# Optimization experiments

Measured on AMD Instinct MI355X. Metric: run time of the kernel, lower is better.

Reference implementation:

```python
import jax, jax.numpy as jnp
import numpy as np

B, G, D, N_HEADS, FFN, L = 16, 2048, 256, 8, 1024, 4
HEAD_DIM = D // N_HEADS
EPS_LN = 1e-5
MASK_TOKEN = -10.0
REE_BASE = 100.0


def setup_inputs() -> dict:
    key = jax.random.key(0)
    ks = jax.random.split(key, 20)
    s = 0.02
    inp = {
        'x': jax.random.normal(ks[0], (B, G), jnp.float32),
        'gene_emb': jax.random.normal(ks[1], (G, D), jnp.float32) * s,
        'inv_freq': (1.0 / REE_BASE ** (jnp.arange(0, D, 2, dtype=jnp.float32) / D)),
        'Wq': jax.random.normal(ks[2], (L, D, D), jnp.float32) * s,
        'bq': jnp.zeros((L, D), jnp.float32),
        'Wk': jax.random.normal(ks[3], (L, D, D), jnp.float32) * s,
        'bk': jnp.zeros((L, D), jnp.float32),
        'Wv': jax.random.normal(ks[4], (L, D, D), jnp.float32) * s,
        'bv': jnp.zeros((L, D), jnp.float32),
        'ln1_g': jnp.ones((L, D), jnp.float32),
        'ln1_b': jnp.zeros((L, D), jnp.float32),
        'ln2_g': jnp.ones((L, D), jnp.float32),
        'ln2_b': jnp.zeros((L, D), jnp.float32),
        'WU': jax.random.normal(ks[5], (L, D, FFN), jnp.float32) * s,
        'bU': jnp.zeros((L, FFN), jnp.float32),
        'WV': jax.random.normal(ks[6], (L, FFN, D), jnp.float32) * s,
        'bV': jnp.zeros((L, D), jnp.float32),
        'Wout': jax.random.normal(ks[7], (D, 1), jnp.float32) * s,
        'bout': jnp.zeros((1,), jnp.float32),
    }
    return inp


def layernorm(x, g, b):
    m = x.mean(-1, keepdims=True)
    v = ((x - m) ** 2).mean(-1, keepdims=True)
    return (x - m) / jnp.sqrt(v + EPS_LN) * g + b


def causal_linear_attention(q, k, v):
    # q, k already feature-mapped ('sqr'); shapes [B, S, H, dh]
    b, s, h, dh = q.shape
    qs, ks_, vs = (jnp.moveaxis(t, 1, 0) for t in (q, k, v))  # [S,B,H,dh]
    num0 = jnp.zeros((b, h, dh, dh), q.dtype)
    den0 = jnp.zeros((b, h, dh), q.dtype)

    def step(carry, qkv):
        num_s, den_s = carry
        qt, kt, vt = qkv
        num_s = num_s + jnp.einsum('bhf,bhd->bhfd', kt, vt)
        den_s = den_s + kt
        num = jnp.einsum('bhf,bhfd->bhd', qt, num_s)
        den = jnp.einsum('bhf,bhf->bh', qt, den_s)
        return (num_s, den_s), num / (den[..., None] + 1e-16)

    _, out = jax.lax.scan(step, (num0, den0), (qs, ks_, vs))  # [S,B,H,dh]
    return jnp.moveaxis(out, 0, 1).reshape(b, s, h * dh)


def reference(x, gene_emb, inv_freq, Wq, bq, Wk, bk, Wv, bv,
              ln1_g, ln1_b, ln2_g, ln2_b, WU, bU, WV, bV, Wout, bout):
    b, g = x.shape
    # Rotary Expression Embedding
    freqs = x[..., None] * inv_freq  # [B,G,D/2]
    emb = jnp.concatenate([jnp.sin(freqs), jnp.cos(freqs)], axis=-1)  # [B,G,D]
    emb = jnp.where((x == MASK_TOKEN)[..., None], 0.0, emb)
    h = gene_emb[None] + emb  # [B,G,D]

    for l in range(Wq.shape[0]):
        hn = layernorm(h, ln1_g[l], ln1_b[l])  # pre-LN (on_gptln=True)
        q = (hn @ Wq[l] + bq[l]).reshape(b, g, N_HEADS, HEAD_DIM) ** 2
        k = (hn @ Wk[l] + bk[l]).reshape(b, g, N_HEADS, HEAD_DIM) ** 2
        v = (hn @ Wv[l] + bv[l]).reshape(b, g, N_HEADS, HEAD_DIM)
        h = h + causal_linear_attention(q, k, v)
        hn2 = layernorm(h, ln2_g[l], ln2_b[l])
        h = h + jax.nn.gelu(hn2 @ WU[l] + bU[l], approximate=False) @ WV[l] + bV[l]
    return (h @ Wout + bout).squeeze(-1)  # [B,G]
```

## Files before the change

kernel.cpp:

```cpp
#include <hip/hip_runtime.h>
#include <math.h>


#define GG 2048
#define DD 256
#define NROWS 32768
#define NC 32
#define CS 64

typedef __attribute__((ext_vector_type(8))) short bf16x8;
typedef __attribute__((ext_vector_type(4))) float f32x4;

__device__ __forceinline__ short f2bf(float f) {
  union { float f; unsigned u; } v; v.f = f;
  unsigned r = v.u + 0x7FFFu + ((v.u >> 16) & 1u);
  return (short)(r >> 16);
}
__device__ __forceinline__ float bf2f(short s) {
  union { unsigned u; float f; } v; v.u = ((unsigned)(unsigned short)s) << 16;
  return v.f;
}
__device__ __forceinline__ void gld16(const short* g, short* l) {
  __builtin_amdgcn_global_load_lds(
      (const __attribute__((address_space(1))) void*)g,
      (__attribute__((address_space(3))) void*)l, 16, 0, 0);
}
__device__ __forceinline__ float fast_gelu(float x) {
  float y = 1.595769122f * (x + 0.044715f * x * x * x);
  return x / (1.0f + __expf(-y));
}

__global__ __launch_bounds__(256) void embed_kernel(
    const float* __restrict__ x, const float* __restrict__ ge,
    const float* __restrict__ invf, float* __restrict__ h) {
  int bg = blockIdx.x * 4 + (threadIdx.x >> 6);
  int g = bg & (GG - 1);
  int lane = threadIdx.x & 63;
  float xv = x[bg];
  int d = lane * 4;
  float4 e;
  if (lane < 32) {
    float4 f = *(const float4*)&invf[d];
    e.x = sinf(xv * f.x); e.y = sinf(xv * f.y);
    e.z = sinf(xv * f.z); e.w = sinf(xv * f.w);
  } else {
    float4 f = *(const float4*)&invf[d - 128];
    e.x = cosf(xv * f.x); e.y = cosf(xv * f.y);
    e.z = cosf(xv * f.z); e.w = cosf(xv * f.w);
  }
  if (xv == -10.0f) { e.x = 0.f; e.y = 0.f; e.z = 0.f; e.w = 0.f; }
  float4 gv = *(const float4*)&ge[(size_t)g * DD + d];
  float4 o; o.x = gv.x + e.x; o.y = gv.y + e.y; o.z = gv.z + e.z; o.w = gv.w + e.w;
  *(float4*)&h[(size_t)bg * DD + d] = o;
}

__global__ __launch_bounds__(256) void ln_tiled(
    const float* __restrict__ h, const float* __restrict__ gamma,
    const float* __restrict__ beta, short* __restrict__ outT) {
  __shared__ float mean_s[32], rstd_s[32];
  __shared__ float gls[256], bls[256];
  int r0 = blockIdx.x * 32;
  int tid = threadIdx.x;
  gls[tid] = gamma[tid]; bls[tid] = beta[tid];
  {
    int row = tid >> 3, seg = tid & 7;
    const float4* hp = (const float4*)(h + (size_t)(r0 + row) * DD + seg * 32);
    float s = 0.f, s2 = 0.f;
#pragma unroll
    for (int i = 0; i < 8; ++i) {
      float4 v = hp[i];
      s += v.x + v.y + v.z + v.w;
      s2 += v.x * v.x + v.y * v.y + v.z * v.z + v.w * v.w;
    }
    s += __shfl_xor(s, 1); s += __shfl_xor(s, 2); s += __shfl_xor(s, 4);
    s2 += __shfl_xor(s2, 1); s2 += __shfl_xor(s2, 2); s2 += __shfl_xor(s2, 4);
    if (seg == 0) {
      float mn = s * (1.0f / 256.0f);
      mean_s[row] = mn;
      rstd_s[row] = rsqrtf(s2 * (1.0f / 256.0f) - mn * mn + 1e-5f);
    }
  }
  __syncthreads();
  int row = tid & 31, kc8 = (tid >> 5) & 3, half = tid >> 7;
  float mn = mean_s[row], rs = rstd_s[row];
  size_t hrow = (size_t)(r0 + row) * DD;
  int trow = (r0 & 127) + row;
  short* tb = outT + (size_t)(r0 >> 7) * 8 * 4096 + (kc8 * 128 + trow) * 8;
#pragma unroll
  for (int j = 0; j < 4; ++j) {
    int kb = half * 4 + j;
    int k0 = kb * 32 + kc8 * 8;
    float4 x0 = *(const float4*)&h[hrow + k0];
    float4 x1 = *(const float4*)&h[hrow + k0 + 4];
    float4 g0 = *(const float4*)&gls[k0], g1 = *(const float4*)&gls[k0 + 4];
    float4 b0 = *(const float4*)&bls[k0], b1 = *(const float4*)&bls[k0 + 4];
    bf16x8 aw;
    aw[0] = f2bf((x0.x - mn) * rs * g0.x + b0.x);
    aw[1] = f2bf((x0.y - mn) * rs * g0.y + b0.y);
    aw[2] = f2bf((x0.z - mn) * rs * g0.z + b0.z);
    aw[3] = f2bf((x0.w - mn) * rs * g0.w + b0.w);
    aw[4] = f2bf((x1.x - mn) * rs * g1.x + b1.x);
    aw[5] = f2bf((x1.y - mn) * rs * g1.y + b1.y);
    aw[6] = f2bf((x1.z - mn) * rs * g1.z + b1.z);
    aw[7] = f2bf((x1.w - mn) * rs * g1.w + b1.w);
    *(bf16x8*)&tb[(size_t)kb * 4096] = aw;
  }
}

__global__ __launch_bounds__(256) void prep_weights(
    const float* __restrict__ Wq, const float* __restrict__ Wk,
    const float* __restrict__ Wv, const float* __restrict__ WU,
    const float* __restrict__ WV,
    short* __restrict__ TQ, short* __restrict__ TK, short* __restrict__ TV,
    short* __restrict__ TU, short* __restrict__ TVd) {
  int zz = blockIdx.z, l = blockIdx.y;
  const float* src; short* dst; int Kd, Nd;
  if (zz == 0) { src = Wq; dst = TQ; Kd = 256; Nd = 256; }
  else if (zz == 1) { src = Wk; dst = TK; Kd = 256; Nd = 256; }
  else if (zz == 2) { src = Wv; dst = TV; Kd = 256; Nd = 256; }
  else if (zz == 3) { src = WU; dst = TU; Kd = 256; Nd = 1024; }
  else { src = WV; dst = TVd; Kd = 1024; Nd = 256; }
  int tot = Kd * Nd;
  int e = blockIdx.x * 256 + threadIdx.x;
  if (e >= tot) return;
  int t = e >> 12;
  int cslot = (e >> 3) & 511;
  int elem = e & 7;
  int kc8 = cslot >> 7, rn = cslot & 127;
  int nKb = Kd >> 5;
  int nt = t / nKb, kb = t - nt * nKb;
  int n = nt * 128 + rn, k = kb * 32 + kc8 * 8 + elem;
  dst[(size_t)l * tot + e] = f2bf(src[(size_t)l * tot + (size_t)k * Nd + n]);
}

__global__ __launch_bounds__(256) void gemm_qkv(
    const short* __restrict__ A, const short* __restrict__ B0,
    const short* __restrict__ B1, const short* __restrict__ B2,
    const float* __restrict__ bias0, const float* __restrict__ bias1,
    const float* __restrict__ bias2,
    short* __restrict__ o0, short* __restrict__ o1, short* __restrict__ o2) {
  __shared__ __align__(16) short L[24576];
  constexpr int nIter = 8;
  int z = blockIdx.z;
  const short* Bt = (z == 0) ? B0 : (z == 1) ? B1 : B2;
  const float* bias = (z == 0) ? bias0 : (z == 1) ? bias1 : bias2;
  short* outz = (z == 0) ? o0 : (z == 1) ? o1 : o2;
  int m0 = blockIdx.x * 128, n0 = blockIdx.y * 128;
  int tid = threadIdx.x;
  int lane = tid & 63, w = tid >> 6;
  int q = lane >> 4, r = lane & 15;
  int wm = (w >> 1) * 64, wn = (w & 1) * 64;
  const short* At = A + (size_t)blockIdx.x * nIter * 4096;
  const short* Btl = Bt + (size_t)blockIdx.y * nIter * 4096;
  f32x4 vzero = {0.f, 0.f, 0.f, 0.f};
  f32x4 acc[4][4];
#pragma unroll
  for (int i = 0; i < 4; ++i)
#pragma unroll
    for (int j = 0; j < 4; ++j) acc[i][j] = vzero;

  int c0 = tid * 8, c1 = (tid + 256) * 8;
#pragma unroll
  for (int g = 0; g < 3; ++g) {
    gld16(At + g * 4096 + c0, &L[g * 4096 + c0]);
    gld16(At + g * 4096 + c1, &L[g * 4096 + c1]);
    gld16(Btl + g * 4096 + c0, &L[12288 + g * 4096 + c0]);
    gld16(Btl + g * 4096 + c1, &L[12288 + g * 4096 + c1]);
  }
  int abase = (q * 128 + wm + r) * 8;
  int bbase = (q * 128 + wn + r) * 8;

#pragma unroll
  for (int gi = 0; gi < nIter; ++gi) {
    const int rem = nIter - 1 - gi;
    if (rem >= 2)      __builtin_amdgcn_s_waitcnt(0x0f78);
    else if (rem == 1) __builtin_amdgcn_s_waitcnt(0x0f74);
    else               __builtin_amdgcn_s_waitcnt(0x0f70);
    __builtin_amdgcn_s_barrier();
    const int cur = gi % 3;
    const short* Asc = &L[cur * 4096];
    const short* Bsc = &L[12288 + cur * 4096];
    bf16x8 af[4], bfr[4];
#pragma unroll
    for (int mt = 0; mt < 4; ++mt)
      af[mt] = *(const bf16x8*)&Asc[abase + mt * 16 * 8];
#pragma unroll
    for (int nt = 0; nt < 4; ++nt)
      bfr[nt] = *(const bf16x8*)&Bsc[bbase + nt * 16 * 8];
#pragma unroll
    for (int mt = 0; mt < 4; ++mt)
#pragma unroll
      for (int nt = 0; nt < 4; ++nt)
        acc[mt][nt] = __builtin_amdgcn_mfma_f32_16x16x32_bf16(bfr[nt], af[mt], acc[mt][nt], 0, 0, 0);
    __builtin_amdgcn_s_waitcnt(0xc07f);
    __builtin_amdgcn_s_barrier();
    if (gi + 3 < nIter) {
      size_t kn = (size_t)(gi + 3) * 4096;
      gld16(At + kn + c0, &L[cur * 4096 + c0]);
      gld16(At + kn + c1, &L[cur * 4096 + c1]);
      gld16(Btl + kn + c0, &L[12288 + cur * 4096 + c0]);
      gld16(Btl + kn + c1, &L[12288 + cur * 4096 + c1]);
    }
  }

  float4 bias4[4];
#pragma unroll
  for (int nt = 0; nt < 4; ++nt) bias4[nt] = *(const float4*)&bias[n0 + wn + nt * 16 + q * 4];
  short* T = L;
#pragma unroll
  for (int mt = 0; mt < 4; ++mt) {
    int ml = wm + mt * 16 + r;
#pragma unroll
    for (int nt = 0; nt < 4; ++nt) {
      f32x4 v = acc[mt][nt];
      v[0] += bias4[nt].x; v[1] += bias4[nt].y; v[2] += bias4[nt].z; v[3] += bias4[nt].w;
      if (z < 2) { v[0] *= v[0]; v[1] *= v[1]; v[2] *= v[2]; v[3] *= v[3]; }
      short4 pk; pk.x = f2bf(v[0]); pk.y = f2bf(v[1]); pk.z = f2bf(v[2]); pk.w = f2bf(v[3]);
      *(short4*)&T[ml * 132 + wn + nt * 16 + q * 4] = pk;
    }
  }
  __syncthreads();
#pragma unroll
  for (int t2 = 0; t2 < 2; ++t2) {
    int task = tid + t2 * 256;
    int row = task & 127, hl = task >> 7;
    size_t obase = ((size_t)((n0 >> 5) + hl) * NROWS + m0 + row) * 32;
#pragma unroll
    for (int j = 0; j < 4; ++j)
      *(bf16x8*)&outz[obase + j * 8] = *(const bf16x8*)&T[row * 132 + hl * 32 + j * 8];
  }
}

__global__ __launch_bounds__(256, 2) void ffn_fused(
    const short* __restrict__ hnT, const short* __restrict__ TU,
    const short* __restrict__ TVd,
    const float* __restrict__ bU, const float* __restrict__ bV,
    float* __restrict__ h) {
  __shared__ __align__(16) short S[21248];
  short* MID = &S[12288];
  int tid = threadIdx.x;
  int lane = tid & 63, w = tid >> 6;
  int q = lane >> 4, r = lane & 15;
  int m0 = blockIdx.x * 64;
  int wm1 = (w >> 1) * 32, wn1 = (w & 1) * 64;
  int wm2 = w * 16;
  const short* Abase = hnT + (size_t)(m0 >> 7) * 32768 +
                       ((tid >> 6) * 128 + (m0 & 127) + (tid & 63)) * 8;
  int c0 = tid * 8, c1 = (tid + 256) * 8;

  f32x4 vzero = {0.f, 0.f, 0.f, 0.f};
  f32x4 acc2[16];
#pragma unroll
  for (int i = 0; i < 16; ++i) acc2[i] = vzero;

  int ab1 = (q * 64 + wm1 + r) * 8;
  int bb1 = (q * 128 + wn1 + r) * 8;
  int ab2 = (wm2 + r) * 136 + q * 8;

  for (int f = 0; f < 8; ++f) {
    const short* Ub = TU + (size_t)f * 8 * 4096;
#pragma unroll
    for (int g = 0; g < 2; ++g) {
      gld16(Abase + g * 4096, &S[g * 2048 + tid * 8]);
      gld16(Ub + g * 4096 + c0, &S[4096 + g * 4096 + c0]);
      gld16(Ub + g * 4096 + c1, &S[4096 + g * 4096 + c1]);
    }
    f32x4 acc1[2][4];
#pragma unroll
    for (int i = 0; i < 2; ++i)
#pragma unroll
      for (int j = 0; j < 4; ++j) acc1[i][j] = vzero;
#pragma unroll
    for (int gi = 0; gi < 8; ++gi) {
      if (gi < 7) __builtin_amdgcn_s_waitcnt(0x0f73);
      else        __builtin_amdgcn_s_waitcnt(0x0f70);
      __builtin_amdgcn_s_barrier();
      const int cur = gi & 1;
      const short* Asc = &S[cur * 2048];
      const short* Bsc = &S[4096 + cur * 4096];
      bf16x8 af[2], bfr[4];
#pragma unroll
      for (int mt = 0; mt < 2; ++mt)
        af[mt] = *(const bf16x8*)&Asc[ab1 + mt * 16 * 8];
#pragma unroll
      for (int nt = 0; nt < 4; ++nt)
        bfr[nt] = *(const bf16x8*)&Bsc[bb1 + nt * 16 * 8];
#pragma unroll
      for (int mt = 0; mt < 2; ++mt)
#pragma unroll
        for (int nt = 0; nt < 4; ++nt)
          acc1[mt][nt] = __builtin_amdgcn_mfma_f32_16x16x32_bf16(bfr[nt], af[mt], acc1[mt][nt], 0, 0, 0);
      __builtin_amdgcn_s_waitcnt(0xc07f);
      __builtin_amdgcn_s_barrier();
      if (gi + 2 < 8) {
        size_t kn = (size_t)(gi + 2) * 4096;
        gld16(Abase + kn, &S[cur * 2048 + tid * 8]);
        gld16(Ub + kn + c0, &S[4096 + cur * 4096 + c0]);
        gld16(Ub + kn + c1, &S[4096 + cur * 4096 + c1]);
      }
    }
#pragma unroll
    for (int mt = 0; mt < 2; ++mt) {
      int ml = wm1 + mt * 16 + r;
#pragma unroll
      for (int nt = 0; nt < 4; ++nt) {
        int fl = wn1 + nt * 16 + q * 4;
        float4 bu4 = *(const float4*)&bU[f * 128 + fl];
        f32x4 v = acc1[mt][nt];
        v[0] = fast_gelu(v[0] + bu4.x); v[1] = fast_gelu(v[1] + bu4.y);
        v[2] = fast_gelu(v[2] + bu4.z); v[3] = fast_gelu(v[3] + bu4.w);
        short4 pk; pk.x = f2bf(v[0]); pk.y = f2bf(v[1]); pk.z = f2bf(v[2]); pk.w = f2bf(v[3]);
        *(short4*)&MID[ml * 136 + fl] = pk;
      }
    }
#pragma unroll
    for (int kb2 = 0; kb2 < 4; ++kb2) {
      const short* Vb0 = TVd + (size_t)(4 * f + kb2) * 4096;
      const short* Vb1 = Vb0 + (size_t)32 * 4096;
      gld16(Vb0 + c0, &S[4096 + c0]);
      gld16(Vb0 + c1, &S[4096 + c1]);
      gld16(Vb1 + c0, &S[8192 + c0]);
      gld16(Vb1 + c1, &S[8192 + c1]);
      __builtin_amdgcn_s_waitcnt(0x0070);
      __builtin_amdgcn_s_barrier();
      bf16x8 af1 = *(const bf16x8*)&MID[ab2 + kb2 * 32];
#pragma unroll
      for (int nt = 0; nt < 16; ++nt) {
        int tile = nt >> 3, nl = nt & 7;
        bf16x8 bfr = *(const bf16x8*)&S[4096 + tile * 4096 + (q * 128 + nl * 16 + r) * 8];
        acc2[nt] = __builtin_amdgcn_mfma_f32_16x16x32_bf16(bfr, af1, acc2[nt], 0, 0, 0);
      }
      __builtin_amdgcn_s_waitcnt(0xc07f);
      __builtin_amdgcn_s_barrier();
    }
  }

  float* TF = (float*)S;
  float4 bv4[16];
#pragma unroll
  for (int nt = 0; nt < 16; ++nt) bv4[nt] = *(const float4*)&bV[nt * 16 + q * 4];
#pragma unroll
  for (int half = 0; half < 2; ++half) {
    __syncthreads();
#pragma unroll
    for (int nt8 = 0; nt8 < 8; ++nt8) {
      int nt = half * 8 + nt8;
      f32x4 v = acc2[nt];
      v[0] += bv4[nt].x; v[1] += bv4[nt].y; v[2] += bv4[nt].z; v[3] += bv4[nt].w;
      *(f32x4*)&TF[(wm2 + r) * 132 + nt8 * 16 + q * 4] = v;
    }
    __syncthreads();
    int row = tid >> 2, seg = tid & 3;
    size_t hoff = (size_t)(m0 + row) * DD + half * 128 + seg * 32;
#pragma unroll
    for (int j = 0; j < 8; ++j) {
      float4 add = *(const float4*)&TF[row * 132 + seg * 32 + j * 4];
      float4 cur4 = *(float4*)&h[hoff + j * 4];
      cur4.x += add.x; cur4.y += add.y; cur4.z += add.z; cur4.w += add.w;
      *(float4*)&h[hoff + j * 4] = cur4;
    }
  }
}

__global__ __launch_bounds__(256) void attn_chunk_kv(
    const short* __restrict__ Kb, const short* __restrict__ Vb,
    float* __restrict__ St, float* __restrict__ Zc) {
  __shared__ short Kt[4][32 * 72];
  __shared__ short Vt[4][32 * 72];
  int wid = threadIdx.x >> 6;
  int blk = blockIdx.x * 4 + wid;
  int c = blk & (NC - 1), bh = blk >> 5;
  int b = bh >> 3, hh = bh & 7;
  int lane = threadIdx.x & 63, q = lane >> 4, r = lane & 15;
  size_t rowbase = ((size_t)hh * NROWS + b * GG + c * CS + lane) * 32;
#pragma unroll
  for (int j = 0; j < 4; ++j) {
    bf16x8 kv = *(const bf16x8*)&Kb[rowbase + j * 8];
    bf16x8 vv = *(const bf16x8*)&Vb[rowbase + j * 8];
#pragma unroll
    for (int e = 0; e < 8; ++e) {
      Kt[wid][(j * 8 + e) * 72 + lane] = kv[e];
      Vt[wid][(j * 8 + e) * 72 + lane] = vv[e];
    }
  }
  __syncthreads();
  f32x4 vzero = {0.f, 0.f, 0.f, 0.f};
  f32x4 acc[2][2];
#pragma unroll
  for (int i = 0; i < 2; ++i)
#pragma unroll
    for (int j = 0; j < 2; ++j) acc[i][j] = vzero;
#pragma unroll
  for (int ks = 0; ks < 2; ++ks) {
    bf16x8 afr[2], bfr[2];
#pragma unroll
    for (int mt = 0; mt < 2; ++mt) afr[mt] = *(const bf16x8*)&Kt[wid][(mt * 16 + r) * 72 + ks * 32 + q * 8];
#pragma unroll
    for (int nt = 0; nt < 2; ++nt) bfr[nt] = *(const bf16x8*)&Vt[wid][(nt * 16 + r) * 72 + ks * 32 + q * 8];
#pragma unroll
    for (int mt = 0; mt < 2; ++mt)
#pragma unroll
      for (int nt = 0; nt < 2; ++nt)
        acc[mt][nt] = __builtin_amdgcn_mfma_f32_16x16x32_bf16(afr[mt], bfr[nt], acc[mt][nt], 0, 0, 0);
  }
  float* stp = St + ((size_t)bh * NC + c) * 1024;
#pragma unroll
  for (int mt = 0; mt < 2; ++mt)
#pragma unroll
    for (int nt = 0; nt < 2; ++nt)
      *(f32x4*)&stp[(nt * 16 + r) * 32 + mt * 16 + q * 4] = acc[mt][nt];
  if (lane < 32) {
    float s = 0.f;
#pragma unroll
    for (int j = 0; j < 8; ++j) {
      bf16x8 kr = *(const bf16x8*)&Kt[wid][lane * 72 + j * 8];
#pragma unroll
      for (int e = 0; e < 8; ++e) s += bf2f(kr[e]);
    }
    Zc[((size_t)bh * NC + c) * 32 + lane] = s;
  }
}

__global__ __launch_bounds__(1024) void attn_prefix(float* __restrict__ St, float* __restrict__ Zc) {
  int bh = blockIdx.x, i = threadIdx.x;
  float run = 0.f;
  float* p = St + (size_t)bh * NC * 1024 + i;
#pragma unroll
  for (int c = 0; c < NC; ++c) { float t = p[(size_t)c * 1024]; p[(size_t)c * 1024] = run; run += t; }
  if (i < 32) {
    float rz = 0.f;
    float* pz = Zc + (size_t)bh * NC * 32 + i;
#pragma unroll
    for (int c = 0; c < NC; ++c) { float t = pz[c * 32]; pz[c * 32] = rz; rz += t; }
  }
}

__global__ __launch_bounds__(256) void attn_intra(
    const short* __restrict__ Qb, const short* __restrict__ Kb,
    const short* __restrict__ Vb, const float* __restrict__ St,
    const float* __restrict__ Zc, float* __restrict__ h) {
  __shared__ short P[4][64 * 72];
  __shared__ short Vt[4][32 * 72];
  __shared__ float den[4][64];
  int wid = threadIdx.x >> 6;
  int blk = blockIdx.x * 4 + wid;
  int c = blk & (NC - 1), bh = blk >> 5;
  int b = bh >> 3, hh = bh & 7;
  int lane = threadIdx.x & 63, q = lane >> 4, r = lane & 15;
  size_t hrow0 = (size_t)b * GG + c * CS;
  size_t qrow0 = (size_t)hh * NROWS + b * GG + c * CS;

  const float* zp = Zc + ((size_t)bh * NC + c) * 32;
  float qz = 0.f;
  {
    size_t qoff = (qrow0 + lane) * 32;
#pragma unroll
    for (int j = 0; j < 4; ++j) {
      bf16x8 qv = *(const bf16x8*)&Qb[qoff + j * 8];
#pragma unroll
      for (int e = 0; e < 8; ++e) qz += bf2f(qv[e]) * zp[j * 8 + e];
    }
  }
  den[wid][lane] = qz;
  {
    size_t voff = (qrow0 + lane) * 32;
#pragma unroll
    for (int j = 0; j < 4; ++j) {
      bf16x8 vv = *(const bf16x8*)&Vb[voff + j * 8];
#pragma unroll
      for (int e = 0; e < 8; ++e) Vt[wid][(j * 8 + e) * 72 + lane] = vv[e];
    }
  }
  bf16x8 ak[4], bqf[4];
#pragma unroll
  for (int t4 = 0; t4 < 4; ++t4) {
    ak[t4]  = *(const bf16x8*)&Kb[(qrow0 + t4 * 16 + r) * 32 + q * 8];
    bqf[t4] = *(const bf16x8*)&Qb[(qrow0 + t4 * 16 + r) * 32 + q * 8];
  }
  f32x4 vzero = {0.f, 0.f, 0.f, 0.f};
  f32x4 pacc[4][4];
#pragma unroll
  for (int mt = 0; mt < 4; ++mt)
#pragma unroll
    for (int nt = 0; nt < 4; ++nt)
      pacc[mt][nt] = __builtin_amdgcn_mfma_f32_16x16x32_bf16(ak[mt], bqf[nt], vzero, 0, 0, 0);

  float rs[4] = {0.f, 0.f, 0.f, 0.f};
#pragma unroll
  for (int nt = 0; nt < 4; ++nt) {
    int t = nt * 16 + r;
#pragma unroll
    for (int mt = 0; mt < 4; ++mt) {
      short4 pk;
#pragma unroll
      for (int rr = 0; rr < 4; ++rr) {
        int s = mt * 16 + q * 4 + rr;
        float pv = (s <= t) ? pacc[mt][nt][rr] : 0.f;
        rs[nt] += pv;
        ((short*)&pk)[rr] = f2bf(pv);
      }
      *(short4*)&P[wid][t * 72 + mt * 16 + q * 4] = pk;
    }
  }
#pragma unroll
  for (int nt = 0; nt < 4; ++nt) {
    rs[nt] += __shfl_xor(rs[nt], 16);
    rs[nt] += __shfl_xor(rs[nt], 32);
  }
  __syncthreads();
  if (lane < 16) {
#pragma unroll
    for (int nt = 0; nt < 4; ++nt) den[wid][nt * 16 + lane] += rs[nt];
  }
  __syncthreads();

  f32x4 oacc[4][2];
#pragma unroll
  for (int mt = 0; mt < 4; ++mt)
#pragma unroll
    for (int nt2 = 0; nt2 < 2; ++nt2) oacc[mt][nt2] = vzero;
  const float* stp = St + ((size_t)bh * NC + c) * 1024;
#pragma unroll
  for (int nt2 = 0; nt2 < 2; ++nt2) {
    float4 s0 = *(const float4*)&stp[(nt2 * 16 + r) * 32 + q * 8];
    float4 s1 = *(const float4*)&stp[(nt2 * 16 + r) * 32 + q * 8 + 4];
    bf16x8 bs;
    bs[0] = f2bf(s0.x); bs[1] = f2bf(s0.y); bs[2] = f2bf(s0.z); bs[3] = f2bf(s0.w);
    bs[4] = f2bf(s1.x); bs[5] = f2bf(s1.y); bs[6] = f2bf(s1.z); bs[7] = f2bf(s1.w);
#pragma unroll
    for (int mt = 0; mt < 4; ++mt)
      oacc[mt][nt2] = __builtin_amdgcn_mfma_f32_16x16x32_bf16(bqf[mt], bs, oacc[mt][nt2], 0, 0, 0);
  }
#pragma unroll
  for (int ks = 0; ks < 2; ++ks) {
    bf16x8 ap[4];
#pragma unroll
    for (int mt = 0; mt < 4; ++mt)
      ap[mt] = *(const bf16x8*)&P[wid][(mt * 16 + r) * 72 + ks * 32 + q * 8];
#pragma unroll
    for (int nt2 = 0; nt2 < 2; ++nt2) {
      bf16x8 bv_ = *(const bf16x8*)&Vt[wid][(nt2 * 16 + r) * 72 + ks * 32 + q * 8];
#pragma unroll
      for (int mt = 0; mt < 4; ++mt)
        oacc[mt][nt2] = __builtin_amdgcn_mfma_f32_16x16x32_bf16(ap[mt], bv_, oacc[mt][nt2], 0, 0, 0);
    }
  }
#pragma unroll
  for (int mt = 0; mt < 4; ++mt) {
#pragma unroll
    for (int rr = 0; rr < 4; ++rr) {
      int t = mt * 16 + q * 4 + rr;
      float inv = 1.0f / (den[wid][t] + 1e-16f);
#pragma unroll
      for (int nt2 = 0; nt2 < 2; ++nt2) {
        int d = nt2 * 16 + r;
        size_t off = (hrow0 + t) * DD + hh * 32 + d;
        h[off] += oacc[mt][nt2][rr] * inv;
      }
    }
  }
}

__global__ __launch_bounds__(256) void out_proj(
    const float* __restrict__ h, const float* __restrict__ Wout,
    const float* __restrict__ bout, float* __restrict__ out) {
  int row = blockIdx.x * 4 + (threadIdx.x >> 6);
  int lane = threadIdx.x & 63;
  float4 a = *(const float4*)&h[(size_t)row * DD + lane * 4];
  float4 w = *(const float4*)&Wout[lane * 4];
  float s = a.x * w.x + a.y * w.y + a.z * w.z + a.w * w.w;
#pragma unroll
  for (int o = 1; o < 64; o <<= 1) s += __shfl_xor(s, o);
  if (lane == 0) out[row] = s + bout[0];
}

extern "C" void kernel_launch(void* const* d_in, const int* in_sizes, int n_in,
                              void* d_out, int out_size, void* d_ws, size_t ws_size,
                              hipStream_t stream) {
  const float* x    = (const float*)d_in[0];
  const float* ge   = (const float*)d_in[1];
  const float* invf = (const float*)d_in[2];
  const float* Wq   = (const float*)d_in[3];
  const float* bq   = (const float*)d_in[4];
  const float* Wk   = (const float*)d_in[5];
  const float* bk   = (const float*)d_in[6];
  const float* Wv   = (const float*)d_in[7];
  const float* bv   = (const float*)d_in[8];
  const float* ln1g = (const float*)d_in[9];
  const float* ln1b = (const float*)d_in[10];
  const float* ln2g = (const float*)d_in[11];
  const float* ln2b = (const float*)d_in[12];
  const float* WU   = (const float*)d_in[13];
  const float* bU   = (const float*)d_in[14];
  const float* WV   = (const float*)d_in[15];
  const float* bV   = (const float*)d_in[16];
  const float* Wout = (const float*)d_in[17];
  const float* bout = (const float*)d_in[18];
  float* out = (float*)d_out;

  char* ws = (char*)d_ws;
  float* h   = (float*)(ws + 0);
  short* hn  = (short*)(ws + 33554432);
  char*  R   = ws + 50331648;
  short* qb  = (short*)(R + 0);
  short* kb  = (short*)(R + 16777216);
  short* vb  = (short*)(R + 33554432);
  float* St  = (float*)(R + 50331648);
  float* Zc  = (float*)(R + 67108864);
  char*  WT  = R + 67633152;
  short* TQ  = (short*)(WT + 0);
  short* TK  = (short*)(WT + 524288);
  short* TVq = (short*)(WT + 1048576);
  short* TU  = (short*)(WT + 1572864);
  short* TVd = (short*)(WT + 3670016);

  prep_weights<<<dim3(1024, 4, 5), 256, 0, stream>>>(Wq, Wk, Wv, WU, WV, TQ, TK, TVq, TU, TVd);
  embed_kernel<<<NROWS / 4, 256, 0, stream>>>(x, ge, invf, h);

  for (int l = 0; l < 4; ++l) {
    ln_tiled<<<NROWS / 32, 256, 0, stream>>>(h, ln1g + l * 256, ln1b + l * 256, hn);
    gemm_qkv<<<dim3(256, 2, 3), 256, 0, stream>>>(
        hn, TQ + l * 65536, TK + l * 65536, TVq + l * 65536,
        bq + l * 256, bk + l * 256, bv + l * 256, qb, kb, vb);
    attn_chunk_kv<<<1024, 256, 0, stream>>>(kb, vb, St, Zc);
    attn_prefix<<<128, 1024, 0, stream>>>(St, Zc);
    attn_intra<<<1024, 256, 0, stream>>>(qb, kb, vb, St, Zc, h);
    ln_tiled<<<NROWS / 32, 256, 0, stream>>>(h, ln2g + l * 256, ln2b + l * 256, hn);
    ffn_fused<<<NROWS / 64, 256, 0, stream>>>(
        hn, TU + l * 262144, TVd + l * 262144,
        bU + l * 1024, bV + l * 256, h);
  }
  out_proj<<<NROWS / 4, 256, 0, stream>>>(h, Wout, bout, out);
}
```

Measured before the change: 833.1 us.

## Triple-buffer second FFN GEMM weight tiles and relayout MID for MFMA reads

```diff
diff --git a/kernel.cpp b/kernel.cpp
--- a/kernel.cpp
+++ b/kernel.cpp
@@ -236,7 +236,7 @@
     const short* __restrict__ TVd,
     const float* __restrict__ bU, const float* __restrict__ bV,
     float* __restrict__ h) {
-  __shared__ __align__(16) short S[21248];
+  __shared__ __align__(16) short S[20480];
   short* MID = &S[12288];
   int tid = threadIdx.x;
   int lane = tid & 63, w = tid >> 6;
@@ -255,7 +255,7 @@
 
   int ab1 = (q * 64 + wm1 + r) * 8;
   int bb1 = (q * 128 + wn1 + r) * 8;
-  int ab2 = (wm2 + r) * 136 + q * 8;
+  int ab2 = (q * 64 + wm2 + r) * 8;
 
   for (int f = 0; f < 8; ++f) {
     const short* Ub = TU + (size_t)f * 8 * 4096;
@@ -310,28 +310,41 @@
         v[0] = fast_gelu(v[0] + bu4.x); v[1] = fast_gelu(v[1] + bu4.y);
         v[2] = fast_gelu(v[2] + bu4.z); v[3] = fast_gelu(v[3] + bu4.w);
         short4 pk; pk.x = f2bf(v[0]); pk.y = f2bf(v[1]); pk.z = f2bf(v[2]); pk.w = f2bf(v[3]);
-        *(short4*)&MID[ml * 136 + fl] = pk;
+        int kb2w = fl >> 5, kc8w = (fl >> 3) & 3, el = fl & 7;
+        *(short4*)&MID[kb2w * 2048 + (kc8w * 64 + ml) * 8 + el] = pk;
       }
     }
-#pragma unroll
-    for (int kb2 = 0; kb2 < 4; ++kb2) {
-      const short* Vb0 = TVd + (size_t)(4 * f + kb2) * 4096;
-      const short* Vb1 = Vb0 + (size_t)32 * 4096;
-      gld16(Vb0 + c0, &S[4096 + c0]);
-      gld16(Vb0 + c1, &S[4096 + c1]);
-      gld16(Vb1 + c0, &S[8192 + c0]);
-      gld16(Vb1 + c1, &S[8192 + c1]);
-      __builtin_amdgcn_s_waitcnt(0x0070);
+    {
+      const short* V0 = TVd + (size_t)(4 * f + 0) * 4096;
+      const short* V1 = TVd + (size_t)(4 * f + 1) * 4096;
+      gld16(V0 + c0, &S[c0]);
+      gld16(V0 + c1, &S[c1]);
+      gld16(V1 + c0, &S[4096 + c0]);
+      gld16(V1 + c1, &S[4096 + c1]);
+    }
+#pragma unroll
+    for (int i = 0; i < 8; ++i) {
+      if (i == 0)     __builtin_amdgcn_s_waitcnt(0x0072);
+      else if (i < 7) __builtin_amdgcn_s_waitcnt(0x0f72);
+      else            __builtin_amdgcn_s_waitcnt(0x0f70);
       __builtin_amdgcn_s_barrier();
-      bf16x8 af1 = *(const bf16x8*)&MID[ab2 + kb2 * 32];
-#pragma unroll
-      for (int nt = 0; nt < 16; ++nt) {
-        int tile = nt >> 3, nl = nt & 7;
-        bf16x8 bfr = *(const bf16x8*)&S[4096 + tile * 4096 + (q * 128 + nl * 16 + r) * 8];
-        acc2[nt] = __builtin_amdgcn_mfma_f32_16x16x32_bf16(bfr, af1, acc2[nt], 0, 0, 0);
+      const int t = i >> 2, kb2 = i & 3;
+      const short* Bsc = &S[(i % 3) * 4096];
+      bf16x8 af1 = *(const bf16x8*)&MID[kb2 * 2048 + ab2];
+#pragma unroll
+      for (int nl = 0; nl < 8; ++nl) {
+        bf16x8 bfr = *(const bf16x8*)&Bsc[(q * 128 + nl * 16 + r) * 8];
+        acc2[t * 8 + nl] = __builtin_amdgcn_mfma_f32_16x16x32_bf16(bfr, af1, acc2[t * 8 + nl], 0, 0, 0);
       }
       __builtin_amdgcn_s_waitcnt(0xc07f);
       __builtin_amdgcn_s_barrier();
+      if (i + 2 < 8) {
+        int j = i + 2;
+        const short* Vb = TVd + ((size_t)(4 * f + (j & 3)) + (size_t)(j >> 2) * 32) * 4096;
+        short* dst = &S[(j % 3) * 4096];
+        gld16(Vb + c0, dst + c0);
+        gld16(Vb + c1, dst + c1);
+      }
     }
   }
 
```

Result: faster. 800.3 us (-3.9%).
